# Kernel tuning notes

Hardware: AMD Instinct MI355X
Metric: run time of the kernel (lower is better)

Reference implementation:

```python
import jax, jax.numpy as jnp
import numpy as np

N_NODES = 100000
N_EDGES = 1600000
F_IN = 32
F_OUT = 32


def setup_inputs() -> dict:
    key = jax.random.key(0)
    k_x, k_r, k_c, k_v, k_w, k_b = jax.random.split(key, 6)
    x = jax.random.normal(k_x, (N_NODES, F_IN), dtype=jnp.float32)
    edge_rows = jnp.sort(jax.random.randint(k_r, (N_EDGES,), 0, N_NODES, dtype=jnp.int32))
    edge_cols = jax.random.randint(k_c, (N_EDGES,), 0, N_NODES, dtype=jnp.int32)
    edge_vals = jax.random.uniform(k_v, (N_EDGES,), dtype=jnp.float32)
    # nn.Linear params: weight [out, in], bias [out]
    bound = 1.0 / np.sqrt(F_IN)
    W = jax.random.uniform(k_w, (F_OUT, F_IN), minval=-bound, maxval=bound, dtype=jnp.float32)
    b = jax.random.uniform(k_b, (F_OUT,), minval=-bound, maxval=bound, dtype=jnp.float32)
    return {"x": x, "edge_rows": edge_rows, "edge_cols": edge_cols,
            "edge_vals": edge_vals, "W": W, "b": b}


def reference(x, edge_rows, edge_cols, edge_vals, W, b):
    # adj @ x  (COO spmm): gather source features, scale by edge weight,
    # scatter-add into destination rows.
    msgs = x[edge_cols] * edge_vals[:, None]                 # [E, F_in]
    agg = jax.ops.segment_sum(msgs, edge_rows,
                              num_segments=x.shape[0],
                              indices_are_sorted=True)       # [N, F_in]
    # linear + relu: agg @ W.T + b
    return jax.nn.relu(agg @ W.T + b)                        # [N, F_out]
```

## Files before the change

kernel.cpp:

```cpp
#include <hip/hip_runtime.h>

#define F 32

typedef __attribute__((ext_vector_type(8))) unsigned short us8;
typedef __attribute__((ext_vector_type(4))) unsigned short us4;
typedef __attribute__((ext_vector_type(4))) float f4;
typedef __attribute__((ext_vector_type(8))) __bf16 bf8;

static __device__ __forceinline__ unsigned short f2bf(float f) {
    unsigned int u = __float_as_uint(f);
    u += 0x7FFF + ((u >> 16) & 1);
    return (unsigned short)(u >> 16);
}
static __device__ __forceinline__ float bf2f(unsigned short s) {
    return __uint_as_float(((unsigned int)s) << 16);
}

__global__ __launch_bounds__(256) void prologue_kernel(
    const float* __restrict__ x, const float* __restrict__ W,
    const int* __restrict__ rows,
    unsigned short* __restrict__ y, int* __restrict__ ptr,
    int N, int E, int nxw) {
    int b = blockIdx.x;
    int t = threadIdx.x;
    if (b < nxw) {
        int lane = t & 63;
        int n0 = (b * 4 + (t >> 6)) * 16;
        if (n0 >= N) return;
        int m  = lane & 15;
        int kb = lane >> 4;
        int k0 = kb * 8;

        int ra = n0 + m; if (ra > N - 1) ra = N - 1;
        const f4* __restrict__ xr = (const f4*)(x + (size_t)ra * F + k0);
        f4 xa = xr[0], xb = xr[1];
        float fx[8] = {xa.x, xa.y, xa.z, xa.w, xb.x, xb.y, xb.z, xb.w};
        bf8 Ah, Al;
        #pragma unroll
        for (int i = 0; i < 8; ++i) {
            __bf16 h = (__bf16)fx[i];
            Ah[i] = h;
            Al[i] = (__bf16)(fx[i] - (float)h);
        }

        const f4* __restrict__ w0 = (const f4*)(W + (size_t)m * F + k0);
        const f4* __restrict__ w1 = (const f4*)(W + (size_t)(m + 16) * F + k0);
        f4 wa = w0[0], wb = w0[1], wc = w1[0], wd = w1[1];
        float fw0[8] = {wa.x, wa.y, wa.z, wa.w, wb.x, wb.y, wb.z, wb.w};
        float fw1[8] = {wc.x, wc.y, wc.z, wc.w, wd.x, wd.y, wd.z, wd.w};
        bf8 B0h, B0l, B1h, B1l;
        #pragma unroll
        for (int i = 0; i < 8; ++i) {
            __bf16 h0 = (__bf16)fw0[i];
            B0h[i] = h0;
            B0l[i] = (__bf16)(fw0[i] - (float)h0);
            __bf16 h1 = (__bf16)fw1[i];
            B1h[i] = h1;
            B1l[i] = (__bf16)(fw1[i] - (float)h1);
        }

        f4 acc0 = {0.f, 0.f, 0.f, 0.f}, acc1 = {0.f, 0.f, 0.f, 0.f};
        acc0 = __builtin_amdgcn_mfma_f32_16x16x32_bf16(Ah, B0h, acc0, 0, 0, 0);
        acc0 = __builtin_amdgcn_mfma_f32_16x16x32_bf16(Ah, B0l, acc0, 0, 0, 0);
        acc0 = __builtin_amdgcn_mfma_f32_16x16x32_bf16(Al, B0h, acc0, 0, 0, 0);
        acc1 = __builtin_amdgcn_mfma_f32_16x16x32_bf16(Ah, B1h, acc1, 0, 0, 0);
        acc1 = __builtin_amdgcn_mfma_f32_16x16x32_bf16(Ah, B1l, acc1, 0, 0, 0);
        acc1 = __builtin_amdgcn_mfma_f32_16x16x32_bf16(Al, B1h, acc1, 0, 0, 0);

        int mr = n0 + kb * 4;
        #pragma unroll
        for (int r = 0; r < 4; ++r) {
            int row = mr + r;
            if (row < N) {
                y[(size_t)row * F + m]      = f2bf(acc0[r]);
                y[(size_t)row * F + m + 16] = f2bf(acc1[r]);
            }
        }
    } else {
        int e = (b - nxw) * 256 + t;
        if (e > E) return;
        int prev = (e == 0) ? -1 : rows[e - 1];
        int cur  = (e == E) ? N  : rows[e];
        for (int r = prev + 1; r <= cur; ++r) ptr[r] = e;
    }
}

__global__ __launch_bounds__(256) void gnn_kernel(
    const unsigned short* __restrict__ y,
    const int*   __restrict__ cols,
    const float* __restrict__ vals,
    const int*   __restrict__ row_ptr,
    const float* __restrict__ bias,
    float*       __restrict__ out, int N) {
    int t = threadIdx.x;
    int lane = t & 63;
    int g = lane >> 3;
    int l = lane & 7;
    int n = (blockIdx.x * 4 + (t >> 6)) * 8 + g;
    int start = 0, end = 0;
    if (n < N) { start = row_ptr[n]; end = row_ptr[n + 1]; }

    const us4* __restrict__ y4 = (const us4*)y;

    float a0[4], a1[4];
    #pragma unroll
    for (int i = 0; i < 4; ++i) { a0[i] = 0.f; a1[i] = 0.f; }

    int lim = end - 1; if (lim < 0) lim = 0;

    int cc[8]; float vv[8];
    #pragma unroll
    for (int k = 0; k < 8; ++k) {
        int ek = start + k;
        int ec = (ek < end) ? ek : lim;
        cc[k] = cols[ec];
        vv[k] = vals[ec];
    }

    for (int e = start; e < end; e += 8) {
        int c[8]; float v[8];
        #pragma unroll
        for (int k = 0; k < 8; ++k) {
            c[k] = cc[k];
            v[k] = (e + k < end) ? vv[k] : 0.0f;
        }
        #pragma unroll
        for (int k = 0; k < 8; ++k) {
            int ek = e + 8 + k;
            int ec = (ek < end) ? ek : lim;
            cc[k] = cols[ec];
            vv[k] = vals[ec];
        }
        us4 r[8];
        #pragma unroll
        for (int k = 0; k < 8; ++k) r[k] = y4[(size_t)c[k] * 8 + l];
        #pragma unroll
        for (int k = 0; k < 8; ++k) {
            float* a = (k & 1) ? a1 : a0;
            #pragma unroll
            for (int i = 0; i < 4; ++i)
                a[i] = fmaf(bf2f(r[k][i]), v[k], a[i]);
        }
    }

    if (n < N) {
        const f4* __restrict__ b4 = (const f4*)bias;
        f4 bb = b4[l];
        f4 o;
        o.x = fmaxf(a0[0] + a1[0] + bb.x, 0.f);
        o.y = fmaxf(a0[1] + a1[1] + bb.y, 0.f);
        o.z = fmaxf(a0[2] + a1[2] + bb.z, 0.f);
        o.w = fmaxf(a0[3] + a1[3] + bb.w, 0.f);
        f4* op = (f4*)(out + (size_t)n * F + l * 4);
        __builtin_nontemporal_store(o, op);
    }
}

__global__ __launch_bounds__(256) void gnn_fp32_kernel(
    const float* __restrict__ x,
    const int*   __restrict__ rows,
    const int*   __restrict__ cols,
    const float* __restrict__ vals,
    const float* __restrict__ W,
    const float* __restrict__ bias,
    float*       __restrict__ out,
    int N, int E) {
    __shared__ float Wt[F * F];
    __shared__ float bS[F];
    int t = threadIdx.x;
    for (int i = t; i < F * F; i += 256)
        Wt[(i & 31) * F + (i >> 5)] = W[i];
    if (t < F) bS[t] = bias[t];
    __syncthreads();
    int lane = t & 63;
    int n = blockIdx.x * 4 + (t >> 6);
    if (n >= N) return;
    int g = lane >> 3, l = lane & 7;
    int target = n + (lane >> 5);
    int lo = 0, hi = E;
    while (lo < hi) { int mid = (lo + hi) >> 1; if (rows[mid] < target) lo = mid + 1; else hi = mid; }
    int start = __shfl(lo, 0), end = __shfl(lo, 32);
    const float4* __restrict__ x4 = (const float4*)x;
    float4 acc0 = {0,0,0,0}, acc1 = {0,0,0,0};
    for (int e0 = start; e0 < end; e0 += 16) {
        int ea = e0 + g, eb = ea + 8;
        if (ea < end) { int c = cols[ea]; float v = vals[ea]; float4 xr = x4[c * 8 + l];
            acc0.x = fmaf(xr.x, v, acc0.x); acc0.y = fmaf(xr.y, v, acc0.y);
            acc0.z = fmaf(xr.z, v, acc0.z); acc0.w = fmaf(xr.w, v, acc0.w); }
        if (eb < end) { int c = cols[eb]; float v = vals[eb]; float4 xr = x4[c * 8 + l];
            acc1.x = fmaf(xr.x, v, acc1.x); acc1.y = fmaf(xr.y, v, acc1.y);
            acc1.z = fmaf(xr.z, v, acc1.z); acc1.w = fmaf(xr.w, v, acc1.w); }
    }
    acc0.x += acc1.x; acc0.y += acc1.y; acc0.z += acc1.z; acc0.w += acc1.w;
    #pragma unroll
    for (int m = 8; m < 64; m <<= 1) {
        acc0.x += __shfl_xor(acc0.x, m); acc0.y += __shfl_xor(acc0.y, m);
        acc0.z += __shfl_xor(acc0.z, m); acc0.w += __shfl_xor(acc0.w, m);
    }
    float comp[4] = {acc0.x, acc0.y, acc0.z, acc0.w};
    int fo = lane & 31;
    float o = bS[fo];
    #pragma unroll
    for (int fi = 0; fi < F; ++fi)
        o = fmaf(__shfl(comp[fi & 3], fi >> 2), Wt[fi * F + fo], o);
    if (lane < F) out[n * F + fo] = fmaxf(o, 0.0f);
}

extern "C" void kernel_launch(void* const* d_in, const int* in_sizes, int n_in,
                              void* d_out, int out_size, void* d_ws, size_t ws_size,
                              hipStream_t stream) {
    const float* x    = (const float*)d_in[0];
    const int*   rows = (const int*)  d_in[1];
    const int*   cols = (const int*)  d_in[2];
    const float* vals = (const float*)d_in[3];
    const float* W    = (const float*)d_in[4];
    const float* bias = (const float*)d_in[5];
    float*       out  = (float*)d_out;

    int N = in_sizes[0] / F;
    int E = in_sizes[1];

    size_t rp_bytes = (size_t)(N + 1) * sizeof(int);
    size_t y_off    = (rp_bytes + 255) & ~(size_t)255;
    size_t need     = y_off + (size_t)N * F * sizeof(unsigned short);

    if (ws_size >= need) {
        int* row_ptr = (int*)d_ws;
        unsigned short* y = (unsigned short*)((char*)d_ws + y_off);
        int nxw  = (N + 63) / 64;
        int ncsr = (E + 1 + 255) / 256;
        prologue_kernel<<<nxw + ncsr, 256, 0, stream>>>(x, W, rows, y, row_ptr, N, E, nxw);
        gnn_kernel<<<(N + 31) / 32, 256, 0, stream>>>(y, cols, vals, row_ptr, bias, out, N);
    } else {
        gnn_fp32_kernel<<<(N + 3) / 4, 256, 0, stream>>>(
            x, rows, cols, vals, W, bias, out, N, E);
    }
}
```

Baseline: 111.7 us.

## Fuse CSR build, SpMM and linear into one kernel with binary-search row bounds

```diff
diff --git a/kernel.cpp b/kernel.cpp
--- a/kernel.cpp
+++ b/kernel.cpp
@@ -2,105 +2,36 @@
 
 #define F 32
 
-typedef __attribute__((ext_vector_type(8))) unsigned short us8;
-typedef __attribute__((ext_vector_type(4))) unsigned short us4;
 typedef __attribute__((ext_vector_type(4))) float f4;
-typedef __attribute__((ext_vector_type(8))) __bf16 bf8;
 
-static __device__ __forceinline__ unsigned short f2bf(float f) {
-    unsigned int u = __float_as_uint(f);
-    u += 0x7FFF + ((u >> 16) & 1);
-    return (unsigned short)(u >> 16);
-}
-static __device__ __forceinline__ float bf2f(unsigned short s) {
-    return __uint_as_float(((unsigned int)s) << 16);
-}
-
-__global__ __launch_bounds__(256) void prologue_kernel(
-    const float* __restrict__ x, const float* __restrict__ W,
-    const int* __restrict__ rows,
-    unsigned short* __restrict__ y, int* __restrict__ ptr,
-    int N, int E, int nxw) {
-    int b = blockIdx.x;
-    int t = threadIdx.x;
-    if (b < nxw) {
-        int lane = t & 63;
-        int n0 = (b * 4 + (t >> 6)) * 16;
-        if (n0 >= N) return;
-        int m  = lane & 15;
-        int kb = lane >> 4;
-        int k0 = kb * 8;
-
-        int ra = n0 + m; if (ra > N - 1) ra = N - 1;
-        const f4* __restrict__ xr = (const f4*)(x + (size_t)ra * F + k0);
-        f4 xa = xr[0], xb = xr[1];
-        float fx[8] = {xa.x, xa.y, xa.z, xa.w, xb.x, xb.y, xb.z, xb.w};
-        bf8 Ah, Al;
-        #pragma unroll
-        for (int i = 0; i < 8; ++i) {
-            __bf16 h = (__bf16)fx[i];
-            Ah[i] = h;
-            Al[i] = (__bf16)(fx[i] - (float)h);
-        }
-
-        const f4* __restrict__ w0 = (const f4*)(W + (size_t)m * F + k0);
-        const f4* __restrict__ w1 = (const f4*)(W + (size_t)(m + 16) * F + k0);
-        f4 wa = w0[0], wb = w0[1], wc = w1[0], wd = w1[1];
-        float fw0[8] = {wa.x, wa.y, wa.z, wa.w, wb.x, wb.y, wb.z, wb.w};
-        float fw1[8] = {wc.x, wc.y, wc.z, wc.w, wd.x, wd.y, wd.z, wd.w};
-        bf8 B0h, B0l, B1h, B1l;
-        #pragma unroll
-        for (int i = 0; i < 8; ++i) {
-            __bf16 h0 = (__bf16)fw0[i];
-            B0h[i] = h0;
-            B0l[i] = (__bf16)(fw0[i] - (float)h0);
-            __bf16 h1 = (__bf16)fw1[i];
-            B1h[i] = h1;
-            B1l[i] = (__bf16)(fw1[i] - (float)h1);
-        }
-
-        f4 acc0 = {0.f, 0.f, 0.f, 0.f}, acc1 = {0.f, 0.f, 0.f, 0.f};
-        acc0 = __builtin_amdgcn_mfma_f32_16x16x32_bf16(Ah, B0h, acc0, 0, 0, 0);
-        acc0 = __builtin_amdgcn_mfma_f32_16x16x32_bf16(Ah, B0l, acc0, 0, 0, 0);
-        acc0 = __builtin_amdgcn_mfma_f32_16x16x32_bf16(Al, B0h, acc0, 0, 0, 0);
-        acc1 = __builtin_amdgcn_mfma_f32_16x16x32_bf16(Ah, B1h, acc1, 0, 0, 0);
-        acc1 = __builtin_amdgcn_mfma_f32_16x16x32_bf16(Ah, B1l, acc1, 0, 0, 0);
-        acc1 = __builtin_amdgcn_mfma_f32_16x16x32_bf16(Al, B1h, acc1, 0, 0, 0);
-
-        int mr = n0 + kb * 4;
-        #pragma unroll
-        for (int r = 0; r < 4; ++r) {
-            int row = mr + r;
-            if (row < N) {
-                y[(size_t)row * F + m]      = f2bf(acc0[r]);
-                y[(size_t)row * F + m + 16] = f2bf(acc1[r]);
-            }
-        }
-    } else {
-        int e = (b - nxw) * 256 + t;
-        if (e > E) return;
-        int prev = (e == 0) ? -1 : rows[e - 1];
-        int cur  = (e == E) ? N  : rows[e];
-        for (int r = prev + 1; r <= cur; ++r) ptr[r] = e;
-    }
-}
-
-__global__ __launch_bounds__(256) void gnn_kernel(
-    const unsigned short* __restrict__ y,
+__global__ __launch_bounds__(256) void gnn_fused_kernel(
+    const float* __restrict__ x,
+    const int*   __restrict__ rows,
     const int*   __restrict__ cols,
     const float* __restrict__ vals,
-    const int*   __restrict__ row_ptr,
+    const float* __restrict__ W,
     const float* __restrict__ bias,
-    float*       __restrict__ out, int N) {
+    float*       __restrict__ out,
+    int N, int E) {
     int t = threadIdx.x;
     int lane = t & 63;
     int g = lane >> 3;
     int l = lane & 7;
-    int n = (blockIdx.x * 4 + (t >> 6)) * 8 + g;
-    int start = 0, end = 0;
-    if (n < N) { start = row_ptr[n]; end = row_ptr[n + 1]; }
+    int n0 = (blockIdx.x * 4 + (t >> 6)) * 8;
+    int n = n0 + g;
 
-    const us4* __restrict__ y4 = (const us4*)y;
+    int target = n0 + (lane < 8 ? lane : 8);
+    if (target > N) target = N;
+    int lo = 0, hi = E;
+    while (lo < hi) {
+        int mid = (lo + hi) >> 1;
+        lo = (rows[mid] < target) ? mid + 1 : lo;
+        hi = (rows[mid] < target) ? hi : mid;
+    }
+    int start = __shfl(lo, g);
+    int end   = __shfl(lo, g + 1);
+
+    const f4* __restrict__ x4 = (const f4*)x;
 
     float a0[4], a1[4];
     #pragma unroll
@@ -131,79 +62,53 @@
             cc[k] = cols[ec];
             vv[k] = vals[ec];
         }
-        us4 r[8];
+        f4 r[8];
         #pragma unroll
-        for (int k = 0; k < 8; ++k) r[k] = y4[(size_t)c[k] * 8 + l];
+        for (int k = 0; k < 8; ++k) r[k] = x4[(size_t)c[k] * 8 + l];
         #pragma unroll
         for (int k = 0; k < 8; ++k) {
             float* a = (k & 1) ? a1 : a0;
             #pragma unroll
             for (int i = 0; i < 4; ++i)
-                a[i] = fmaf(bf2f(r[k][i]), v[k], a[i]);
+                a[i] = fmaf(r[k][i], v[k], a[i]);
+        }
+    }
+
+    float a[4];
+    #pragma unroll
+    for (int i = 0; i < 4; ++i) a[i] = a0[i] + a1[i];
+
+    const f4* __restrict__ W4 = (const f4*)W;
+    const f4* __restrict__ b4 = (const f4*)bias;
+    f4 bb = b4[l];
+    float o[4] = {bb.x, bb.y, bb.z, bb.w};
+
+    int gbase = lane & 56;
+    #pragma unroll
+    for (int j = 0; j < 8; ++j) {
+        float av0 = __shfl(a[0], gbase | j);
+        float av1 = __shfl(a[1], gbase | j);
+        float av2 = __shfl(a[2], gbase | j);
+        float av3 = __shfl(a[3], gbase | j);
+        #pragma unroll
+        for (int i = 0; i < 4; ++i) {
+            f4 wr = W4[(size_t)(4 * l + i) * 8 + j];
+            o[i] = fmaf(av0, wr.x, o[i]);
+            o[i] = fmaf(av1, wr.y, o[i]);
+            o[i] = fmaf(av2, wr.z, o[i]);
+            o[i] = fmaf(av3, wr.w, o[i]);
         }
     }
 
     if (n < N) {
-        const f4* __restrict__ b4 = (const f4*)bias;
-        f4 bb = b4[l];
-        f4 o;
-        o.x = fmaxf(a0[0] + a1[0] + bb.x, 0.f);
-        o.y = fmaxf(a0[1] + a1[1] + bb.y, 0.f);
-        o.z = fmaxf(a0[2] + a1[2] + bb.z, 0.f);
-        o.w = fmaxf(a0[3] + a1[3] + bb.w, 0.f);
+        f4 oo;
+        oo.x = fmaxf(o[0], 0.f);
+        oo.y = fmaxf(o[1], 0.f);
+        oo.z = fmaxf(o[2], 0.f);
+        oo.w = fmaxf(o[3], 0.f);
         f4* op = (f4*)(out + (size_t)n * F + l * 4);
-        __builtin_nontemporal_store(o, op);
+        __builtin_nontemporal_store(oo, op);
     }
-}
-
-__global__ __launch_bounds__(256) void gnn_fp32_kernel(
-    const float* __restrict__ x,
-    const int*   __restrict__ rows,
-    const int*   __restrict__ cols,
-    const float* __restrict__ vals,
-    const float* __restrict__ W,
-    const float* __restrict__ bias,
-    float*       __restrict__ out,
-    int N, int E) {
-    __shared__ float Wt[F * F];
-    __shared__ float bS[F];
-    int t = threadIdx.x;
-    for (int i = t; i < F * F; i += 256)
-        Wt[(i & 31) * F + (i >> 5)] = W[i];
-    if (t < F) bS[t] = bias[t];
-    __syncthreads();
-    int lane = t & 63;
-    int n = blockIdx.x * 4 + (t >> 6);
-    if (n >= N) return;
-    int g = lane >> 3, l = lane & 7;
-    int target = n + (lane >> 5);
-    int lo = 0, hi = E;
-    while (lo < hi) { int mid = (lo + hi) >> 1; if (rows[mid] < target) lo = mid + 1; else hi = mid; }
-    int start = __shfl(lo, 0), end = __shfl(lo, 32);
-    const float4* __restrict__ x4 = (const float4*)x;
-    float4 acc0 = {0,0,0,0}, acc1 = {0,0,0,0};
-    for (int e0 = start; e0 < end; e0 += 16) {
-        int ea = e0 + g, eb = ea + 8;
-        if (ea < end) { int c = cols[ea]; float v = vals[ea]; float4 xr = x4[c * 8 + l];
-            acc0.x = fmaf(xr.x, v, acc0.x); acc0.y = fmaf(xr.y, v, acc0.y);
-            acc0.z = fmaf(xr.z, v, acc0.z); acc0.w = fmaf(xr.w, v, acc0.w); }
-        if (eb < end) { int c = cols[eb]; float v = vals[eb]; float4 xr = x4[c * 8 + l];
-            acc1.x = fmaf(xr.x, v, acc1.x); acc1.y = fmaf(xr.y, v, acc1.y);
-            acc1.z = fmaf(xr.z, v, acc1.z); acc1.w = fmaf(xr.w, v, acc1.w); }
-    }
-    acc0.x += acc1.x; acc0.y += acc1.y; acc0.z += acc1.z; acc0.w += acc1.w;
-    #pragma unroll
-    for (int m = 8; m < 64; m <<= 1) {
-        acc0.x += __shfl_xor(acc0.x, m); acc0.y += __shfl_xor(acc0.y, m);
-        acc0.z += __shfl_xor(acc0.z, m); acc0.w += __shfl_xor(acc0.w, m);
-    }
-    float comp[4] = {acc0.x, acc0.y, acc0.z, acc0.w};
-    int fo = lane & 31;
-    float o = bS[fo];
-    #pragma unroll
-    for (int fi = 0; fi < F; ++fi)
-        o = fmaf(__shfl(comp[fi & 3], fi >> 2), Wt[fi * F + fo], o);
-    if (lane < F) out[n * F + fo] = fmaxf(o, 0.0f);
 }
 
 extern "C" void kernel_launch(void* const* d_in, const int* in_sizes, int n_in,
@@ -220,19 +125,9 @@
     int N = in_sizes[0] / F;
     int E = in_sizes[1];
 
-    size_t rp_bytes = (size_t)(N + 1) * sizeof(int);
-    size_t y_off    = (rp_bytes + 255) & ~(size_t)255;
-    size_t need     = y_off + (size_t)N * F * sizeof(unsigned short);
+    (void)d_ws; (void)ws_size;
 
-    if (ws_size >= need) {
-        int* row_ptr = (int*)d_ws;
-        unsigned short* y = (unsigned short*)((char*)d_ws + y_off);
-        int nxw  = (N + 63) / 64;
-        int ncsr = (E + 1 + 255) / 256;
-        prologue_kernel<<<nxw + ncsr, 256, 0, stream>>>(x, W, rows, y, row_ptr, N, E, nxw);
-        gnn_kernel<<<(N + 31) / 32, 256, 0, stream>>>(y, cols, vals, row_ptr, bias, out, N);
-    } else {
-        gnn_fp32_kernel<<<(N + 3) / 4, 256, 0, stream>>>(
-            x, rows, cols, vals, W, bias, out, N, E);
-    }
+    int nblk = (N + 31) / 32;
+    gnn_fused_kernel<<<nblk, 256, 0, stream>>>(
+        x, rows, cols, vals, W, bias, out, N, E);
 }
```

Measured after the change: 158.6 us. 1.42x slower.

## Split each row's edges across two lane groups with aligned vector index loads

Applied to the files above, without the earlier changes.

```diff
diff --git a/kernel.cpp b/kernel.cpp
--- a/kernel.cpp
+++ b/kernel.cpp
@@ -2,9 +2,9 @@
 
 #define F 32
 
-typedef __attribute__((ext_vector_type(8))) unsigned short us8;
 typedef __attribute__((ext_vector_type(4))) unsigned short us4;
 typedef __attribute__((ext_vector_type(4))) float f4;
+typedef __attribute__((ext_vector_type(4))) int i4;
 typedef __attribute__((ext_vector_type(8))) __bf16 bf8;
 
 static __device__ __forceinline__ unsigned short f2bf(float f) {
@@ -91,45 +91,48 @@
     const float* __restrict__ vals,
     const int*   __restrict__ row_ptr,
     const float* __restrict__ bias,
-    float*       __restrict__ out, int N) {
+    float*       __restrict__ out, int N, int E) {
     int t = threadIdx.x;
     int lane = t & 63;
-    int g = lane >> 3;
+    int p = lane >> 4;
+    int s = (lane >> 3) & 1;
     int l = lane & 7;
-    int n = (blockIdx.x * 4 + (t >> 6)) * 8 + g;
+    int n = (blockIdx.x * 4 + (t >> 6)) * 4 + p;
     int start = 0, end = 0;
     if (n < N) { start = row_ptr[n]; end = row_ptr[n + 1]; }
 
     const us4* __restrict__ y4 = (const us4*)y;
 
-    float a0[4], a1[4];
-    #pragma unroll
-    for (int i = 0; i < 4; ++i) { a0[i] = 0.f; a1[i] = 0.f; }
-
-    int lim = end - 1; if (lim < 0) lim = 0;
-
-    int cc[8]; float vv[8];
-    #pragma unroll
-    for (int k = 0; k < 8; ++k) {
-        int ek = start + k;
-        int ec = (ek < end) ? ek : lim;
-        cc[k] = cols[ec];
-        vv[k] = vals[ec];
-    }
-
-    for (int e = start; e < end; e += 8) {
-        int c[8]; float v[8];
+    float a0[4] = {0.f, 0.f, 0.f, 0.f};
+    float a1[4] = {0.f, 0.f, 0.f, 0.f};
+
+    int firstb = start >> 3;
+    int lastb  = (end - 1) >> 3;
+    for (int b = firstb + s; b <= lastb; b += 2) {
+        int e0 = b << 3;
+        i4 c0, c1; f4 v0, v1;
+        if (e0 + 8 <= E) {
+            c0 = __builtin_nontemporal_load((const i4*)(cols + e0));
+            c1 = __builtin_nontemporal_load((const i4*)(cols + e0 + 4));
+            v0 = __builtin_nontemporal_load((const f4*)(vals + e0));
+            v1 = __builtin_nontemporal_load((const f4*)(vals + e0 + 4));
+        } else {
+            #pragma unroll
+            for (int k = 0; k < 4; ++k) {
+                int ea = e0 + k;     if (ea > E - 1) ea = E - 1;
+                int eb = e0 + 4 + k; if (eb > E - 1) eb = E - 1;
+                c0[k] = cols[ea]; v0[k] = vals[ea];
+                c1[k] = cols[eb]; v1[k] = vals[eb];
+            }
+        }
+        int   c[8] = {c0[0], c0[1], c0[2], c0[3], c1[0], c1[1], c1[2], c1[3]};
+        float v[8] = {v0[0], v0[1], v0[2], v0[3], v1[0], v1[1], v1[2], v1[3]};
         #pragma unroll
         for (int k = 0; k < 8; ++k) {
-            c[k] = cc[k];
-            v[k] = (e + k < end) ? vv[k] : 0.0f;
-        }
-        #pragma unroll
-        for (int k = 0; k < 8; ++k) {
-            int ek = e + 8 + k;
-            int ec = (ek < end) ? ek : lim;
-            cc[k] = cols[ec];
-            vv[k] = vals[ec];
+            int ek = e0 + k;
+            bool valid = (ek >= start) & (ek < end);
+            c[k] = valid ? c[k] : 0;
+            v[k] = valid ? v[k] : 0.0f;
         }
         us4 r[8];
         #pragma unroll
@@ -143,14 +146,21 @@
         }
     }
 
-    if (n < N) {
+    float a[4];
+    #pragma unroll
+    for (int i = 0; i < 4; ++i) {
+        a[i] = a0[i] + a1[i];
+        a[i] += __shfl_xor(a[i], 8);
+    }
+
+    if (n < N && s == 0) {
         const f4* __restrict__ b4 = (const f4*)bias;
         f4 bb = b4[l];
         f4 o;
-        o.x = fmaxf(a0[0] + a1[0] + bb.x, 0.f);
-        o.y = fmaxf(a0[1] + a1[1] + bb.y, 0.f);
-        o.z = fmaxf(a0[2] + a1[2] + bb.z, 0.f);
-        o.w = fmaxf(a0[3] + a1[3] + bb.w, 0.f);
+        o.x = fmaxf(a[0] + bb.x, 0.f);
+        o.y = fmaxf(a[1] + bb.y, 0.f);
+        o.z = fmaxf(a[2] + bb.z, 0.f);
+        o.w = fmaxf(a[3] + bb.w, 0.f);
         f4* op = (f4*)(out + (size_t)n * F + l * 4);
         __builtin_nontemporal_store(o, op);
     }
@@ -230,7 +240,7 @@
         int nxw  = (N + 63) / 64;
         int ncsr = (E + 1 + 255) / 256;
         prologue_kernel<<<nxw + ncsr, 256, 0, stream>>>(x, W, rows, y, row_ptr, N, E, nxw);
-        gnn_kernel<<<(N + 31) / 32, 256, 0, stream>>>(y, cols, vals, row_ptr, bias, out, N);
+        gnn_kernel<<<(N + 15) / 16, 256, 0, stream>>>(y, cols, vals, row_ptr, bias, out, N, E);
     } else {
         gnn_fp32_kernel<<<(N + 3) / 4, 256, 0, stream>>>(
             x, rows, cols, vals, W, bias, out, N, E);
```

New measurement: 114.8 us. 2.7% more time.
